# Performance work log

Hardware: AMD Instinct MI355X
Metric: run time of the kernel (lower is better)

The kernel has to match this reference:

```python
import jax, jax.numpy as jnp
import numpy as np

X_DIM = 362
N_EXPERTS = 3
HIDDEN = [1024, 2048, 2048, 1024]  # layer widths; final layer maps back to X_DIM


def _init_params(key):
    dims = [X_DIM] + HIDDEN + [X_DIM]
    params = {}
    for li in range(len(dims) - 1):
        fan_in = dims[li]
        kW, kb, key = jax.random.split(key, 3)
        bound = 1.0 / np.sqrt(fan_in)
        # stacked over experts: [E, in, out]
        params[f"W{li}"] = jax.random.uniform(kW, (N_EXPERTS, dims[li], dims[li + 1]), jnp.float32, -bound, bound)
        params[f"b{li}"] = jax.random.uniform(kb, (N_EXPERTS, dims[li + 1]), jnp.float32, -bound, bound)
    return params


def setup_inputs() -> dict:
    key = jax.random.key(0)
    kx, kn, ka, kp = jax.random.split(key, 4)
    B = 8192
    inp = {
        "batch_x": jax.random.normal(kx, (B, X_DIM), jnp.float32),
        "batch_next": jax.random.normal(kn, (B, X_DIM), jnp.float32),
        "batch_a": jax.random.randint(ka, (B,), 0, N_EXPERTS, jnp.int64),
    }
    inp.update(_init_params(kp))
    return inp


def _experts_forward(x, W0, b0, W1, b1, W2, b2, W3, b3, W4, b4):
    # Run every expert on the full batch (dense grouped GEMMs), then select.
    # h: [E, B, d]
    h = jax.nn.relu(jnp.einsum("bi,eio->ebo", x, W0) + b0[:, None, :])
    h = jax.nn.relu(jnp.einsum("ebi,eio->ebo", h, W1) + b1[:, None, :])
    h = jax.nn.relu(jnp.einsum("ebi,eio->ebo", h, W2) + b2[:, None, :])
    h = jax.nn.relu(jnp.einsum("ebi,eio->ebo", h, W3) + b3[:, None, :])
    return jnp.einsum("ebi,eio->ebo", h, W4) + b4[:, None, :]  # [E, B, X_DIM]


def reference(batch_x, batch_next, batch_a, W0, b0, W1, b1, W2, b2, W3, b3, W4, b4):
    preds = _experts_forward(batch_x, W0, b0, W1, b1, W2, b2, W3, b3, W4, b4)
    # route: pick each sample's prediction from its action's expert
    pred_next = preds[batch_a, jnp.arange(batch_x.shape[0])]  # [B, X_DIM]
    return jnp.mean((pred_next - batch_next) ** 2)
```

## Files before the change

kernel.cpp:

```cpp
#include <hip/hip_runtime.h>
#include <hip/hip_bf16.h>

#define B_SZ   8192
#define XD     362
#define NEXP   3
#define NTILES 70
#define MP     (NTILES*128)

typedef __bf16 bf16x8 __attribute__((ext_vector_type(8)));
typedef float  f32x4  __attribute__((ext_vector_type(4)));

__device__ __forceinline__ unsigned short f2bf(float f) {
    unsigned u = __float_as_uint(f);
    u += 0x7fffu + ((u >> 16) & 1u);
    return (unsigned short)(u >> 16);
}

__global__ __launch_bounds__(1024) void k_route(const int* __restrict__ a,
                                                int* __restrict__ hdr,
                                                int* __restrict__ row_of) {
    __shared__ int wpre[3][16];
    __shared__ int stot[3];
    int tid = threadIdx.x, lane = tid & 63, w = tid >> 6;
    int ev[8];
    int c0 = 0, c1 = 0, c2 = 0;
#pragma unroll
    for (int j = 0; j < 8; ++j) {
        int e = a[tid * 8 + j];
        ev[j] = e;
        c0 += (e == 0); c1 += (e == 1); c2 += (e == 2);
    }
    int i0 = c0, i1 = c1, i2 = c2;
#pragma unroll
    for (int off = 1; off < 64; off <<= 1) {
        int t0_ = __shfl_up(i0, off, 64);
        int t1_ = __shfl_up(i1, off, 64);
        int t2_ = __shfl_up(i2, off, 64);
        if (lane >= off) { i0 += t0_; i1 += t1_; i2 += t2_; }
    }
    if (lane == 63) { wpre[0][w] = i0; wpre[1][w] = i1; wpre[2][w] = i2; }
    __syncthreads();
    if (tid == 0) {
        int s0 = 0, s1 = 0, s2 = 0;
#pragma unroll
        for (int k = 0; k < 16; ++k) {
            int a0 = wpre[0][k], a1 = wpre[1][k], a2 = wpre[2][k];
            wpre[0][k] = s0; wpre[1][k] = s1; wpre[2][k] = s2;
            s0 += a0; s1 += a1; s2 += a2;
        }
        stot[0] = s0; stot[1] = s1; stot[2] = s2;
    }
    __syncthreads();
    int tot0 = stot[0], tot1 = stot[1], tot2 = stot[2];
    int t0 = ((tot0 + 255) >> 8) << 1;
    int t1 = ((tot1 + 255) >> 8) << 1;
    int t2 = ((tot2 + 255) >> 8) << 1;
    int seg0 = 0, seg1 = t0 * 128, seg2 = (t0 + t1) * 128;
    int nt = t0 + t1 + t2;
    int b0 = seg0 + wpre[0][w] + i0 - c0;
    int b1 = seg1 + wpre[1][w] + i1 - c1;
    int b2 = seg2 + wpre[2][w] + i2 - c2;
#pragma unroll
    for (int j = 0; j < 8; ++j) {
        int e = ev[j];
        int pos = (e == 0) ? b0++ : (e == 1) ? b1++ : b2++;
        row_of[pos] = tid * 8 + j;
    }
    if (tid == 0) {
        hdr[0] = tot0; hdr[1] = tot1; hdr[2] = tot2;
        hdr[6] = seg0; hdr[7] = seg1; hdr[8] = seg2;
        hdr[12] = nt;
        hdr[13] = nt / 2 - 1;
        hdr[16] = 0;
    }
    if (tid < NTILES)
        hdr[32 + tid] = (tid < t0) ? 0 : (tid < t0 + t1) ? 1 : (tid < nt) ? 2 : -1;
    for (int r = tid; r < MP; r += 1024) {
        int pad;
        if (r < seg1)           pad = (r - seg0) >= tot0;
        else if (r < seg2)      pad = (r - seg1) >= tot1;
        else if (r < nt * 128)  pad = (r - seg2) >= tot2;
        else                    pad = 1;
        if (pad) row_of[r] = -1;
    }
}

__global__ void k_gather(const float* __restrict__ x, const int* __restrict__ row_of,
                         unsigned short* __restrict__ xg) {
    int r = blockIdx.x;
    int c = threadIdx.x;
    int orig = row_of[r];
    float v = (orig >= 0 && c < XD) ? x[(size_t)orig * XD + c] : 0.f;
    xg[(size_t)r * 384 + c] = f2bf(v);
}

__device__ __forceinline__ void transpose_tile(const float* __restrict__ We,
                                               unsigned short* __restrict__ Wte,
                                               int K, int N, int Kp,
                                               int kb, int nb, int tx, int ty,
                                               float (*t)[33]) {
#pragma unroll
    for (int j = 0; j < 8; ++j) {
        int k = kb + ty + j * 8, n = nb + tx;
        t[ty + j * 8][tx] = (k < K && n < N) ? We[(size_t)k * N + n] : 0.f;
    }
    __syncthreads();
#pragma unroll
    for (int j = 0; j < 4; ++j) {
        int n = ty + j * 8;
        unsigned int lo = f2bf(t[2 * tx][n]);
        unsigned int hi = f2bf(t[2 * tx + 1][n]);
        *(unsigned int*)&Wte[(size_t)(nb + n) * Kp + kb + 2 * tx] = lo | (hi << 16);
    }
}

__global__ void k_transpose(const float* __restrict__ W, unsigned short* __restrict__ Wt,
                            int K, int N, int Kp, int Np) {
    __shared__ float t[64][33];
    int e  = blockIdx.z;
    int kb = blockIdx.x * 64, nb = blockIdx.y * 32;
    transpose_tile(W + (size_t)e * K * N, Wt + (size_t)e * Np * Kp,
                   K, N, Kp, kb, nb, threadIdx.x, threadIdx.y, t);
}

#define WT_OFF0 0
#define WT_OFF1 1179648u
#define WT_OFF2 7471104u
#define WT_OFF3 20054016u
#define WT_OFF4 26345472u
#define WT_TOTAL 27525120u

__global__ void k_transpose_all(const float* __restrict__ W0, const float* __restrict__ W1,
                                const float* __restrict__ W2, const float* __restrict__ W3,
                                const float* __restrict__ W4, unsigned short* __restrict__ Wt) {
    __shared__ float t[64][33];
    int ti = blockIdx.x, e = blockIdx.z;
    const float* W; int K, N, Kp, kt; unsigned off; int Np;
    if (ti < 192)       { W = W0; K = 362;  N = 1024; Kp = 384;  Np = 1024; kt = 6;  off = WT_OFF0; }
    else if (ti < 1216) { W = W1; K = 1024; N = 2048; Kp = 1024; Np = 2048; kt = 16; off = WT_OFF1; ti -= 192; }
    else if (ti < 3264) { W = W2; K = 2048; N = 2048; Kp = 2048; Np = 2048; kt = 32; off = WT_OFF2; ti -= 1216; }
    else if (ti < 4288) { W = W3; K = 2048; N = 1024; Kp = 2048; Np = 1024; kt = 32; off = WT_OFF3; ti -= 3264; }
    else                { W = W4; K = 1024; N = 362;  Kp = 1024; Np = 384;  kt = 16; off = WT_OFF4; ti -= 4288; }
    int kb = (ti % kt) * 64, nb = (ti / kt) * 32;
    transpose_tile(W + (size_t)e * K * N, Wt + off + (size_t)e * Np * Kp,
                   K, N, Kp, kb, nb, threadIdx.x, threadIdx.y, t);
}

template <int TM, int TN, int WAVES, bool FINAL, bool TAIL, bool SKIPLAST>
__global__ __launch_bounds__(WAVES * 64) void k_gemm(
    const unsigned short* __restrict__ A, int lda,
    const unsigned short* __restrict__ Bt, int K, int Np,
    const float* __restrict__ bias, int nvalid,
    unsigned short* __restrict__ C, int ldc,
    const int* __restrict__ hdr,
    const float* __restrict__ nextv, const int* __restrict__ row_of,
    float* __restrict__ accum)
{
    __shared__ unsigned short As[2][TM * 64];
    __shared__ unsigned short Bs[2][TN * 64];
    __shared__ float red[WAVES];

    constexpr int WGN = TN / 64;
    constexpr int LA  = TM / (WAVES * 8);
    constexpr int LB  = TN / (WAVES * 8);

    int mt128;
    if constexpr (TAIL) {
        mt128 = hdr[13] * 2 + blockIdx.y;
    } else {
        if (SKIPLAST && (int)blockIdx.y >= hdr[13] && TM == 256) return;
        mt128 = blockIdx.y * (TM / 128);
    }
    int e = hdr[32 + mt128];
    if (e < 0) return;
    int row0 = mt128 * 128;
    int n0   = blockIdx.x * TN;

    int tid  = threadIdx.x;
    int wid  = tid >> 6, lane = tid & 63;
    int quad = lane >> 4, l15 = lane & 15;
    int sw   = l15 & 7;
    int wm = (wid / WGN) * 64, wn = (wid % WGN) * 64;

    const unsigned short* Ag = A  + (size_t)row0 * lda;
    const unsigned short* Bg = Bt + (size_t)e * Np * K + (size_t)n0 * K;
    const float* be = bias + (size_t)e * nvalid;

    int srow = lane >> 3;
    int scol = ((lane & 7) ^ srow) * 8;

    f32x4 acc[4][4];
#pragma unroll
    for (int i = 0; i < 4; ++i)
#pragma unroll
        for (int j = 0; j < 4; ++j)
            acc[i][j] = (f32x4){0.f, 0.f, 0.f, 0.f};

#define STAGE(K0, P)                                                              \
    {                                                                             \
        _Pragma("unroll")                                                         \
        for (int ii = 0; ii < LA; ++ii) {                                         \
            int rbase = wid * (TM / WAVES) + ii * 8;                              \
            const unsigned short* gp = Ag + (size_t)(rbase + srow) * lda + (K0) + scol; \
            __builtin_amdgcn_global_load_lds(                                     \
                (const __attribute__((address_space(1))) void*)gp,                \
                (__attribute__((address_space(3))) void*)(As[P] + rbase * 64), 16, 0, 0); \
        }                                                                         \
        _Pragma("unroll")                                                         \
        for (int ii = 0; ii < LB; ++ii) {                                         \
            int rbase = wid * (TN / WAVES) + ii * 8;                              \
            const unsigned short* gp = Bg + (size_t)(rbase + srow) * K + (K0) + scol;   \
            __builtin_amdgcn_global_load_lds(                                     \
                (const __attribute__((address_space(1))) void*)gp,                \
                (__attribute__((address_space(3))) void*)(Bs[P] + rbase * 64), 16, 0, 0); \
        }                                                                         \
    }

#define COMPUTE(P)                                                                \
    {                                                                             \
        _Pragma("unroll")                                                         \
        for (int kh = 0; kh < 2; ++kh) {                                          \
            bf16x8 af[4], bfr[4];                                                 \
            _Pragma("unroll")                                                     \
            for (int f = 0; f < 4; ++f) {                                         \
                int row = wm + f * 16 + l15;                                      \
                af[f] = *(const bf16x8*)(As[P] + row * 64 + (((kh * 4 + quad) ^ sw) << 3)); \
            }                                                                     \
            _Pragma("unroll")                                                     \
            for (int f = 0; f < 4; ++f) {                                         \
                int row = wn + f * 16 + l15;                                      \
                bfr[f] = *(const bf16x8*)(Bs[P] + row * 64 + (((kh * 4 + quad) ^ sw) << 3)); \
            }                                                                     \
            _Pragma("unroll")                                                     \
            for (int fm = 0; fm < 4; ++fm)                                        \
                _Pragma("unroll")                                                 \
                for (int fn = 0; fn < 4; ++fn)                                    \
                    acc[fm][fn] = __builtin_amdgcn_mfma_f32_16x16x32_bf16(        \
                        af[fm], bfr[fn], acc[fm][fn], 0, 0, 0);                   \
        }                                                                         \
    }

    STAGE(0, 0);
    __syncthreads();
    for (int k0 = 0; k0 < K; k0 += 128) {
        if (k0 + 64 < K) STAGE(k0 + 64, 1);
        COMPUTE(0);
        __syncthreads();
        if (k0 + 128 < K) STAGE(k0 + 128, 0);
        COMPUTE(1);
        __syncthreads();
    }
#undef STAGE
#undef COMPUTE

    if constexpr (!FINAL) {
#pragma unroll
        for (int fn = 0; fn < 4; ++fn) {
            int n = n0 + wn + fn * 16 + l15;
            float bv = be[n];
#pragma unroll
            for (int fm = 0; fm < 4; ++fm) {
#pragma unroll
                for (int i = 0; i < 4; ++i) {
                    int r = row0 + wm + fm * 16 + quad * 4 + i;
                    float v = acc[fm][fn][i] + bv;
                    v = v > 0.f ? v : 0.f;
                    C[(size_t)r * ldc + n] = f2bf(v);
                }
            }
        }
    } else {
        float local = 0.f;
#pragma unroll
        for (int fm = 0; fm < 4; ++fm) {
#pragma unroll
            for (int i = 0; i < 4; ++i) {
                int r = row0 + wm + fm * 16 + quad * 4 + i;
                int orig_r = row_of[r];
                if (orig_r >= 0) {
                    const float* nrow = nextv + (size_t)orig_r * XD;
#pragma unroll
                    for (int fn = 0; fn < 4; ++fn) {
                        int n = n0 + wn + fn * 16 + l15;
                        if (n < XD) {
                            float v = acc[fm][fn][i] + be[n];
                            float d = v - nrow[n];
                            local += d * d;
                        }
                    }
                }
            }
        }
        for (int off = 32; off > 0; off >>= 1)
            local += __shfl_down(local, off, 64);
        if (lane == 0) red[wid] = local;
        __syncthreads();
        if (tid == 0) {
            float s = 0.f;
#pragma unroll
            for (int w = 0; w < WAVES; ++w) s += red[w];
            atomicAdd(accum, s);
        }
    }
}

__global__ void k_final(const int* hdr, float* out) {
    if (blockIdx.x == 0 && threadIdx.x == 0) {
        float s = ((const float*)hdr)[16];
        out[0] = s / (float)(B_SZ * XD);
    }
}

extern "C" void kernel_launch(void* const* d_in, const int* in_sizes, int n_in,
                              void* d_out, int out_size, void* d_ws, size_t ws_size,
                              hipStream_t stream) {
    const float* x     = (const float*)d_in[0];
    const float* nextv = (const float*)d_in[1];
    const int*   a     = (const int*)d_in[2];
    const float* W0 = (const float*)d_in[3],  *b0 = (const float*)d_in[4];
    const float* W1 = (const float*)d_in[5],  *b1 = (const float*)d_in[6];
    const float* W2 = (const float*)d_in[7],  *b2 = (const float*)d_in[8];
    const float* W3 = (const float*)d_in[9],  *b3 = (const float*)d_in[10];
    const float* W4 = (const float*)d_in[11], *b4 = (const float*)d_in[12];

    int* hdr    = (int*)d_ws;
    int* row_of = hdr + 128;
    unsigned short* xg = (unsigned short*)(row_of + MP);
    unsigned short* hA = xg + (size_t)MP * 384;
    unsigned short* hB = hA + (size_t)MP * 2048;
    unsigned short* Wt = hB + (size_t)MP * 2048;
    float* accum = (float*)(hdr + 16);

    size_t base = (size_t)(128 + MP) * 4 + (size_t)MP * 384 * 2 + (size_t)MP * 2048 * 2 * 2;
    bool merged = ws_size >= base + (size_t)WT_TOTAL * 2;

    unsigned short *Wt0, *Wt1, *Wt2, *Wt3, *Wt4;
    if (merged) {
        Wt0 = Wt + WT_OFF0; Wt1 = Wt + WT_OFF1; Wt2 = Wt + WT_OFF2;
        Wt3 = Wt + WT_OFF3; Wt4 = Wt + WT_OFF4;
        k_transpose_all<<<dim3(4480, 1, 3), dim3(32, 8), 0, stream>>>(W0, W1, W2, W3, W4, Wt);
    } else {
        Wt0 = Wt1 = Wt2 = Wt3 = Wt4 = Wt;
    }

    k_route <<<1, 1024, 0, stream>>>(a, hdr, row_of);
    k_gather<<<MP, 384, 0, stream>>>(x, row_of, xg);

    if (!merged) k_transpose<<<dim3(6, 32, 3), dim3(32, 8), 0, stream>>>(W0, Wt0, XD, 1024, 384, 1024);
    k_gemm<128, 128, 4, false, false, false><<<dim3(8, NTILES), 256, 0, stream>>>(
        xg, 384, Wt0, 384, 1024, b0, 1024, hA, 1024, hdr, nullptr, nullptr, nullptr);

    if (!merged) k_transpose<<<dim3(16, 64, 3), dim3(32, 8), 0, stream>>>(W1, Wt1, 1024, 2048, 1024, 2048);
    k_gemm<256, 256, 16, false, false, true><<<dim3(8, NTILES / 2), 1024, 0, stream>>>(
        hA, 1024, Wt1, 1024, 2048, b1, 2048, hB, 2048, hdr, nullptr, nullptr, nullptr);
    k_gemm<128, 256, 8, false, true, false><<<dim3(8, 2), 512, 0, stream>>>(
        hA, 1024, Wt1, 1024, 2048, b1, 2048, hB, 2048, hdr, nullptr, nullptr, nullptr);

    if (!merged) k_transpose<<<dim3(32, 64, 3), dim3(32, 8), 0, stream>>>(W2, Wt2, 2048, 2048, 2048, 2048);
    k_gemm<256, 256, 16, false, false, true><<<dim3(8, NTILES / 2), 1024, 0, stream>>>(
        hB, 2048, Wt2, 2048, 2048, b2, 2048, hA, 2048, hdr, nullptr, nullptr, nullptr);
    k_gemm<128, 256, 8, false, true, false><<<dim3(8, 2), 512, 0, stream>>>(
        hB, 2048, Wt2, 2048, 2048, b2, 2048, hA, 2048, hdr, nullptr, nullptr, nullptr);

    if (!merged) k_transpose<<<dim3(32, 32, 3), dim3(32, 8), 0, stream>>>(W3, Wt3, 2048, 1024, 2048, 1024);
    k_gemm<128, 128, 4, false, false, false><<<dim3(8, NTILES), 256, 0, stream>>>(
        hA, 2048, Wt3, 2048, 1024, b3, 1024, hB, 1024, hdr, nullptr, nullptr, nullptr);

    if (!merged) k_transpose<<<dim3(16, 12, 3), dim3(32, 8), 0, stream>>>(W4, Wt4, 1024, XD, 1024, 384);
    k_gemm<128, 128, 4, true, false, false><<<dim3(3, NTILES), 256, 0, stream>>>(
        hB, 1024, Wt4, 1024, 384, b4, XD, nullptr, 0, hdr, nextv, row_of, accum);

    k_final<<<1, 64, 0, stream>>>(hdr, (float*)d_out);
}
```

Baseline: 505.3 us.

## Split-K the tail GEMM tiles and use 256x256 tiles for layer three

The small tail GEMM launches (8x2 blocks) for layers 1-2 are replaced by a 4-way split-K version that writes fp32 partials to workspace, followed by a reduction kernel that adds bias, applies ReLU and converts to bf16. Layer 3 moves from 128x128 tiles to the 256x256 tile path plus a tail kernel, also split-K. The aim is to fill more CUs on the poorly parallel tail and to get more data reuse from bigger tiles. In exchange it adds extra launches and partial-sum traffic, and it depends on enough workspace being available.

New measurement: 487.5 us. -3.5%, faster.

```diff
diff --git a/kernel.cpp b/kernel.cpp
--- a/kernel.cpp
+++ b/kernel.cpp
@@ -146,7 +146,7 @@
                    K, N, Kp, kb, nb, threadIdx.x, threadIdx.y, t);
 }
 
-template <int TM, int TN, int WAVES, bool FINAL, bool TAIL, bool SKIPLAST>
+template <int TM, int TN, int WAVES, bool FINAL, bool TAIL, bool SKIPLAST, int KSPLIT = 1>
 __global__ __launch_bounds__(WAVES * 64) void k_gemm(
     const unsigned short* __restrict__ A, int lda,
     const unsigned short* __restrict__ Bt, int K, int Np,
@@ -188,6 +188,13 @@
 
     int srow = lane >> 3;
     int scol = ((lane & 7) ^ srow) * 8;
+
+    int kbeg = 0, kend = K;
+    if constexpr (KSPLIT > 1) {
+        int kh = K / KSPLIT;
+        kbeg = blockIdx.z * kh;
+        kend = kbeg + kh;
+    }
 
     f32x4 acc[4][4];
 #pragma unroll
@@ -219,17 +226,17 @@
 #define COMPUTE(P)                                                                \
     {                                                                             \
         _Pragma("unroll")                                                         \
-        for (int kh = 0; kh < 2; ++kh) {                                          \
+        for (int kh2 = 0; kh2 < 2; ++kh2) {                                       \
             bf16x8 af[4], bfr[4];                                                 \
             _Pragma("unroll")                                                     \
             for (int f = 0; f < 4; ++f) {                                         \
                 int row = wm + f * 16 + l15;                                      \
-                af[f] = *(const bf16x8*)(As[P] + row * 64 + (((kh * 4 + quad) ^ sw) << 3)); \
+                af[f] = *(const bf16x8*)(As[P] + row * 64 + (((kh2 * 4 + quad) ^ sw) << 3)); \
             }                                                                     \
             _Pragma("unroll")                                                     \
             for (int f = 0; f < 4; ++f) {                                         \
                 int row = wn + f * 16 + l15;                                      \
-                bfr[f] = *(const bf16x8*)(Bs[P] + row * 64 + (((kh * 4 + quad) ^ sw) << 3)); \
+                bfr[f] = *(const bf16x8*)(Bs[P] + row * 64 + (((kh2 * 4 + quad) ^ sw) << 3)); \
             }                                                                     \
             _Pragma("unroll")                                                     \
             for (int fm = 0; fm < 4; ++fm)                                        \
@@ -240,20 +247,34 @@
         }                                                                         \
     }
 
-    STAGE(0, 0);
+    STAGE(kbeg, 0);
     __syncthreads();
-    for (int k0 = 0; k0 < K; k0 += 128) {
-        if (k0 + 64 < K) STAGE(k0 + 64, 1);
+    for (int k0 = kbeg; k0 < kend; k0 += 128) {
+        if (k0 + 64 < kend) STAGE(k0 + 64, 1);
         COMPUTE(0);
         __syncthreads();
-        if (k0 + 128 < K) STAGE(k0 + 128, 0);
+        if (k0 + 128 < kend) STAGE(k0 + 128, 0);
         COMPUTE(1);
         __syncthreads();
     }
 #undef STAGE
 #undef COMPUTE
 
-    if constexpr (!FINAL) {
+    if constexpr (KSPLIT > 1) {
+        float* P = accum + (size_t)blockIdx.z * 256 * Np;
+#pragma unroll
+        for (int fn = 0; fn < 4; ++fn) {
+            int n = n0 + wn + fn * 16 + l15;
+#pragma unroll
+            for (int fm = 0; fm < 4; ++fm) {
+#pragma unroll
+                for (int i = 0; i < 4; ++i) {
+                    int rl = blockIdx.y * 128 + wm + fm * 16 + quad * 4 + i;
+                    P[(size_t)rl * Np + n] = acc[fm][fn][i];
+                }
+            }
+        }
+    } else if constexpr (!FINAL) {
 #pragma unroll
         for (int fn = 0; fn < 4; ++fn) {
             int n = n0 + wn + fn * 16 + l15;
@@ -304,6 +325,22 @@
     }
 }
 
+__global__ void k_tailc(const float* __restrict__ P, const float* __restrict__ bias,
+                        int Np, int KS, unsigned short* __restrict__ C, int ldc,
+                        const int* __restrict__ hdr) {
+    int r = blockIdx.x;
+    int e = hdr[32 + hdr[13] * 2];
+    int row = hdr[13] * 256 + r;
+    const float* be = bias + (size_t)e * Np;
+    for (int n = threadIdx.x; n < Np; n += blockDim.x) {
+        float s = 0.f;
+        for (int z = 0; z < KS; ++z) s += P[((size_t)z * 256 + r) * Np + n];
+        float v = s + be[n];
+        v = v > 0.f ? v : 0.f;
+        C[(size_t)row * ldc + n] = f2bf(v);
+    }
+}
+
 __global__ void k_final(const int* hdr, float* out) {
     if (blockIdx.x == 0 && threadIdx.x == 0) {
         float s = ((const float*)hdr)[16];
@@ -332,7 +369,10 @@
     float* accum = (float*)(hdr + 16);
 
     size_t base = (size_t)(128 + MP) * 4 + (size_t)MP * 384 * 2 + (size_t)MP * 2048 * 2 * 2;
+    const size_t PBYTES = (size_t)4 * 256 * 2048 * 4;
     bool merged = ws_size >= base + (size_t)WT_TOTAL * 2;
+    float* Ppart = (float*)(Wt + WT_TOTAL);
+    bool sk = merged && ws_size >= base + (size_t)WT_TOTAL * 2 + PBYTES;
 
     unsigned short *Wt0, *Wt1, *Wt2, *Wt3, *Wt4;
     if (merged) {
@@ -353,18 +393,38 @@
     if (!merged) k_transpose<<<dim3(16, 64, 3), dim3(32, 8), 0, stream>>>(W1, Wt1, 1024, 2048, 1024, 2048);
     k_gemm<256, 256, 16, false, false, true><<<dim3(8, NTILES / 2), 1024, 0, stream>>>(
         hA, 1024, Wt1, 1024, 2048, b1, 2048, hB, 2048, hdr, nullptr, nullptr, nullptr);
-    k_gemm<128, 256, 8, false, true, false><<<dim3(8, 2), 512, 0, stream>>>(
-        hA, 1024, Wt1, 1024, 2048, b1, 2048, hB, 2048, hdr, nullptr, nullptr, nullptr);
+    if (sk) {
+        k_gemm<128, 256, 8, false, true, false, 4><<<dim3(8, 2, 4), 512, 0, stream>>>(
+            hA, 1024, Wt1, 1024, 2048, b1, 2048, hB, 2048, hdr, nullptr, nullptr, Ppart);
+        k_tailc<<<256, 256, 0, stream>>>(Ppart, b1, 2048, 4, hB, 2048, hdr);
+    } else {
+        k_gemm<128, 256, 8, false, true, false><<<dim3(8, 2), 512, 0, stream>>>(
+            hA, 1024, Wt1, 1024, 2048, b1, 2048, hB, 2048, hdr, nullptr, nullptr, nullptr);
+    }
 
     if (!merged) k_transpose<<<dim3(32, 64, 3), dim3(32, 8), 0, stream>>>(W2, Wt2, 2048, 2048, 2048, 2048);
     k_gemm<256, 256, 16, false, false, true><<<dim3(8, NTILES / 2), 1024, 0, stream>>>(
         hB, 2048, Wt2, 2048, 2048, b2, 2048, hA, 2048, hdr, nullptr, nullptr, nullptr);
-    k_gemm<128, 256, 8, false, true, false><<<dim3(8, 2), 512, 0, stream>>>(
-        hB, 2048, Wt2, 2048, 2048, b2, 2048, hA, 2048, hdr, nullptr, nullptr, nullptr);
+    if (sk) {
+        k_gemm<128, 256, 8, false, true, false, 4><<<dim3(8, 2, 4), 512, 0, stream>>>(
+            hB, 2048, Wt2, 2048, 2048, b2, 2048, hA, 2048, hdr, nullptr, nullptr, Ppart);
+        k_tailc<<<256, 256, 0, stream>>>(Ppart, b2, 2048, 4, hA, 2048, hdr);
+    } else {
+        k_gemm<128, 256, 8, false, true, false><<<dim3(8, 2), 512, 0, stream>>>(
+            hB, 2048, Wt2, 2048, 2048, b2, 2048, hA, 2048, hdr, nullptr, nullptr, nullptr);
+    }
 
     if (!merged) k_transpose<<<dim3(32, 32, 3), dim3(32, 8), 0, stream>>>(W3, Wt3, 2048, 1024, 2048, 1024);
-    k_gemm<128, 128, 4, false, false, false><<<dim3(8, NTILES), 256, 0, stream>>>(
+    k_gemm<256, 256, 16, false, false, true><<<dim3(4, NTILES / 2), 1024, 0, stream>>>(
         hA, 2048, Wt3, 2048, 1024, b3, 1024, hB, 1024, hdr, nullptr, nullptr, nullptr);
+    if (sk) {
+        k_gemm<128, 256, 8, false, true, false, 4><<<dim3(4, 2, 4), 512, 0, stream>>>(
+            hA, 2048, Wt3, 2048, 1024, b3, 1024, hB, 1024, hdr, nullptr, nullptr, Ppart);
+        k_tailc<<<256, 256, 0, stream>>>(Ppart, b3, 1024, 4, hB, 1024, hdr);
+    } else {
+        k_gemm<128, 256, 8, false, true, false><<<dim3(4, 2), 512, 0, stream>>>(
+            hA, 2048, Wt3, 2048, 1024, b3, 1024, hB, 1024, hdr, nullptr, nullptr, nullptr);
+    }
 
     if (!merged) k_transpose<<<dim3(16, 12, 3), dim3(32, 8), 0, stream>>>(W4, Wt4, 1024, XD, 1024, 384);
     k_gemm<128, 128, 4, true, false, false><<<dim3(3, NTILES), 256, 0, stream>>>(
```
